# Performance work log

Measured on AMD Instinct MI355X. Metric: run time of the kernel, lower is better.

Reference implementation:

```python
import jax, jax.numpy as jnp
import numpy as np

D = 512; N_HEAD = 8; D_HEAD = 64; D_INNER = 2048; SEG = 512; N_LAYER = 2; BATCH = 32
NUM_ITEMS = 50000
OMEGA = [2, 3, 4, 5, 7, 11, 21, 50]  # len == N_HEAD, required by multi-scale mask broadcast
EPS = 1e-8
STD = 0.02


def _layer_norm(x, w, b):
    mu = x.mean(-1, keepdims=True)
    var = ((x - mu) ** 2).mean(-1, keepdims=True)
    return (x - mu) / jnp.sqrt(var + EPS) * w + b


def _masks():
    # dir_mask: triu(ones, 1) (reverse=False); ms_mask[i,j,m] per omega band
    dir_mask = jnp.triu(jnp.ones((SEG, SEG), jnp.float32), 1)
    ms = np.stack([np.tri(SEG, SEG, o - 1) != np.tri(SEG, SEG, -o) for o in OMEGA], axis=-1)
    return dir_mask, jnp.asarray(ms)


def _pos_emb():
    freq = jnp.arange(0, D, 2, dtype=jnp.float32)
    inv_freq = 1.0 / jnp.power(10000.0, freq / D)
    pos_seq = jnp.arange(SEG, -SEG, -1.0, dtype=jnp.float32)  # length 2*SEG
    sinusoid = pos_seq[:, None] * inv_freq[None, :]
    return jnp.concatenate([jnp.sin(sinusoid), jnp.cos(sinusoid)], axis=-1)  # (2S, D)


def _rel_shift_bnij(x, klen):
    b, n, i, j2 = x.shape
    x = x.reshape(b, n, j2, i)[:, :, 1:, :].reshape(b, n, i, j2 - 1)
    return x[:, :, :, :klen]


def setup_inputs() -> dict:
    key = jax.random.key(0)
    ks = jax.random.split(key, 16)
    L = N_LAYER
    item_emb = STD * jax.random.normal(ks[0], (NUM_ITEMS + 1, D), jnp.float32)
    item_emb = item_emb.at[0].set(0.0)  # padding_idx=0
    proj = lambda k: STD * jax.random.normal(k, (L, D, N_HEAD, D_HEAD), jnp.float32)
    return {
        "input_ids": jax.random.randint(ks[1], (BATCH, SEG), 0, NUM_ITEMS + 1),
        "input_mask": jnp.zeros((BATCH, SEG), jnp.float32),
        "item_emb": item_emb,
        "Wq": proj(ks[2]), "Wk": proj(ks[3]), "Wv": proj(ks[4]),
        "Wr": proj(ks[5]), "Wo": proj(ks[6]),
        "r_r_bias": STD * jax.random.normal(ks[7], (L, N_HEAD, D_HEAD), jnp.float32),
        "r_w_bias": STD * jax.random.normal(ks[8], (L, N_HEAD, D_HEAD), jnp.float32),
        "ln_attn_w": jnp.ones((L, D), jnp.float32), "ln_attn_b": jnp.zeros((L, D), jnp.float32),
        "W1": STD * jax.random.normal(ks[9], (L, D, D_INNER), jnp.float32),
        "b1": jnp.zeros((L, D_INNER), jnp.float32),
        "W2": STD * jax.random.normal(ks[10], (L, D_INNER, D), jnp.float32),
        "b2": jnp.zeros((L, D), jnp.float32),
        "ln_ff_w": jnp.ones((L, D), jnp.float32), "ln_ff_b": jnp.zeros((L, D), jnp.float32),
    }


def reference(input_ids, input_mask, item_emb, Wq, Wk, Wv, Wr, Wo, r_r_bias, r_w_bias,
              ln_attn_w, ln_attn_b, W1, b1, W2, b2, ln_ff_w, ln_ff_b):
    ids = input_ids.T                      # (S, B)
    im = input_mask.T.astype(jnp.float32)  # (S, B)
    dir_mask, ms_mask = _masks()
    # data_mask: (q,k,b); attn_mask: (q,k,b,n) via multi-scale bands (training path)
    data_mask = im[None, :, :] + im[:, None, :] + dir_mask[:, :, None]
    attn_mask = ((data_mask[:, :, :, None] + (~ms_mask)[:, :, None, :].astype(jnp.float32)) > 0).astype(jnp.float32)
    mask_bnij = jnp.transpose(attn_mask, (2, 3, 0, 1))  # (b,n,i,j)

    h = item_emb[ids]          # (S, B, D)
    pos = _pos_emb()           # (2S, D), shared across batch
    scale = 1.0 / np.sqrt(D_HEAD).astype(np.float32)

    for l in range(N_LAYER):
        k_h = jnp.einsum('ibh,hnd->ibnd', h, Wk[l])
        v_h = jnp.einsum('ibh,hnd->ibnd', h, Wv[l])
        k_r = jnp.einsum('jh,hnd->jnd', pos, Wr[l])   # pos shared across batch
        q_h = jnp.einsum('ibh,hnd->ibnd', h, Wq[l])
        ac = jnp.einsum('ibnd,jbnd->bnij', q_h + r_w_bias[l], k_h)
        bd = jnp.einsum('ibnd,jnd->bnij', q_h + r_r_bias[l], k_r)
        bd = _rel_shift_bnij(bd, SEG)
        attn_score = (ac + bd) * scale - 1e30 * mask_bnij
        attn_prob = jax.nn.softmax(attn_score, axis=3)
        attn_vec = jnp.einsum('bnij,jbnd->ibnd', attn_prob, v_h)
        attn_out = jnp.einsum('ibnd,hnd->ibh', attn_vec, Wo[l])
        h = _layer_norm(attn_out + h, ln_attn_w[l], ln_attn_b[l])
        ff = jax.nn.gelu(h @ W1[l] + b1[l], approximate=False) @ W2[l] + b2[l]
        h = _layer_norm(ff + h, ln_ff_w[l], ln_ff_b[l])

    return jnp.transpose(h, (1, 0, 2))  # (B, S, D)
```

## Files before the change

### kernel.cpp

```cpp
#include <hip/hip_runtime.h>
#include <math.h>


#define S_  512
#define B_  32
#define D_  512
#define NH  8
#define DH  64
#define DI  2048
#define M_  (S_*B_)
#define QKV_LD 1536
#define WL  3407872
#define FP32_ONE 0x3F800000u

typedef unsigned short ushort_t;
typedef __attribute__((ext_vector_type(8))) short short8;
typedef __attribute__((ext_vector_type(4))) float f32x4;

__constant__ int OMEGA_C[8] = {2, 3, 4, 5, 7, 11, 21, 50};

__device__ __forceinline__ float b2f(ushort_t us) {
    return __uint_as_float(((unsigned int)us) << 16);
}
__device__ __forceinline__ ushort_t f2b(float f) {
    unsigned int u = __float_as_uint(f);
    return (ushort_t)((u + 0x7fffu + ((u >> 16) & 1u)) >> 16);
}
__device__ __forceinline__ float ldx(const void* p, size_t idx, bool isbf) {
    return isbf ? b2f(((const ushort_t*)p)[idx]) : ((const float*)p)[idx];
}
__device__ __forceinline__ void async16(const ushort_t* g, ushort_t* l) {
    __builtin_amdgcn_global_load_lds(
        (const __attribute__((address_space(1))) unsigned int*)g,
        (__attribute__((address_space(3))) unsigned int*)l, 16, 0, 0);
}

__device__ __forceinline__ float fast_gelu(float v) {
    float x  = v * 0.7071067811865475f;
    float ax = fabsf(x);
    float t  = __builtin_amdgcn_rcpf(fmaf(0.3275911f, ax, 1.f));
    float p  = fmaf(fmaf(fmaf(fmaf(1.061405429f, t, -1.453152027f),
                              t, 1.421413741f),
                         t, -0.284496736f),
                    t, 0.254829592f) * t;
    float e    = __expf(-ax * ax);
    float erfa = fmaf(-p, e, 1.f);
    float erfx = copysignf(erfa, x);
    return 0.5f * v * (1.f + erfx);
}

#define DPPA(v, ctrl) v += __int_as_float(__builtin_amdgcn_update_dpp(0, __float_as_int(v), ctrl, 0xf, 0xf, true))
__device__ __forceinline__ void dpp_sum64(float& v) {
    DPPA(v, 0x111); DPPA(v, 0x112); DPPA(v, 0x114);
    DPPA(v, 0x118); DPPA(v, 0x142); DPPA(v, 0x143);
}
#define DPPROR(v, ctrl) __int_as_float(__builtin_amdgcn_update_dpp(__float_as_int(v), __float_as_int(v), ctrl, 0xf, 0xf, false))
__device__ __forceinline__ float row16_sum(float v) {
    v += DPPROR(v, 0x128); v += DPPROR(v, 0x124);
    v += DPPROR(v, 0x122); v += DPPROR(v, 0x121);
    return v;
}
__device__ __forceinline__ float row16_max(float v) {
    v = fmaxf(v, DPPROR(v, 0x128)); v = fmaxf(v, DPPROR(v, 0x124));
    v = fmaxf(v, DPPROR(v, 0x122)); v = fmaxf(v, DPPROR(v, 0x121));
    return v;
}
__device__ __forceinline__ float rlane(float v, int l) {
    return __int_as_float(__builtin_amdgcn_readlane(__float_as_int(v), l));
}

__global__ __launch_bounds__(256) void embed_kernel(const int* __restrict__ ids,
                                                    const void* __restrict__ emb,
                                                    ushort_t* __restrict__ h,
                                                    const unsigned int* __restrict__ dtp) {
    const bool isbf = (dtp[0] != FP32_ONE);
    int idx = blockIdx.x * 256 + threadIdx.x;
    int d8 = idx & 63;
    int row = idx >> 6;
    int s = row >> 5, b = row & 31;
    int id = ids[b * S_ + s];
    size_t src = (size_t)id * D_ + d8 * 8;
    if (isbf) {
        *(uint4*)(h + (size_t)row * D_ + d8 * 8) = *(const uint4*)((const ushort_t*)emb + src);
    } else {
        const float* e = (const float*)emb + src;
        float4 a0 = ((const float4*)e)[0], a1 = ((const float4*)e)[1];
        uint4 pk;
        pk.x = (unsigned)f2b(a0.x) | ((unsigned)f2b(a0.y) << 16);
        pk.y = (unsigned)f2b(a0.z) | ((unsigned)f2b(a0.w) << 16);
        pk.z = (unsigned)f2b(a1.x) | ((unsigned)f2b(a1.y) << 16);
        pk.w = (unsigned)f2b(a1.z) | ((unsigned)f2b(a1.w) << 16);
        *(uint4*)(h + (size_t)row * D_ + d8 * 8) = pk;
    }
}

__global__ __launch_bounds__(256) void posemb_kernel(ushort_t* __restrict__ pos) {
    int flat = blockIdx.x * 256 + threadIdx.x;
    int p = flat >> 8, k = flat & 255;
    float inv = expf((float)k * -0.035977892078031f);
    float val = (512.0f - (float)p) * inv;
    pos[p * D_ + k]       = f2b(sinf(val));
    pos[p * D_ + 256 + k] = f2b(cosf(val));
}

__global__ __launch_bounds__(256) void transp_cvt4(
    const void* __restrict__ s0, const void* __restrict__ s1,
    const void* __restrict__ s2, const void* __restrict__ s3,
    ushort_t* __restrict__ wbuf, const unsigned int* __restrict__ dtp) {
    const bool isbf = (dtp[0] != FP32_ONE);
    __shared__ float tt[32][33];
    int z = blockIdx.z, layer = z >> 2, t4 = z & 3;
    const void* srcs[4] = {s0, s1, s2, s3};
    const void* in = srcs[t4];
    size_t inoff = (size_t)layer * 262144;
    ushort_t* out = wbuf + (size_t)layer * WL + (size_t)t4 * 262144;
    int tx = threadIdx.x & 31, ty = threadIdx.x >> 5;
    int n0 = blockIdx.x * 32, k0 = blockIdx.y * 32;
#pragma unroll
    for (int it = 0; it < 4; ++it)
        tt[ty + it * 8][tx] = ldx(in, inoff + (size_t)(k0 + ty + it * 8) * 512 + n0 + tx, isbf);
    __syncthreads();
#pragma unroll
    for (int it = 0; it < 4; ++it)
        out[(size_t)(n0 + ty + it * 8) * 512 + k0 + tx] = f2b(tt[tx][ty + it * 8]);
}

__global__ __launch_bounds__(256) void transp_cvtL(const void* __restrict__ in, size_t perlin,
                                                   ushort_t* __restrict__ wbuf, size_t outoff,
                                                   const unsigned int* __restrict__ dtp,
                                                   int K, int N) {
    const bool isbf = (dtp[0] != FP32_ONE);
    __shared__ float tt[32][33];
    int layer = blockIdx.z;
    size_t inoff = (size_t)layer * perlin;
    ushort_t* out = wbuf + (size_t)layer * WL + outoff;
    int tx = threadIdx.x & 31, ty = threadIdx.x >> 5;
    int n0 = blockIdx.x * 32, k0 = blockIdx.y * 32;
#pragma unroll
    for (int it = 0; it < 4; ++it)
        tt[ty + it * 8][tx] = ldx(in, inoff + (size_t)(k0 + ty + it * 8) * N + n0 + tx, isbf);
    __syncthreads();
#pragma unroll
    for (int it = 0; it < 4; ++it)
        out[(size_t)(n0 + ty + it * 8) * K + k0 + tx] = f2b(tt[tx][ty + it * 8]);
}

__global__ __launch_bounds__(256) void cvtL(const void* __restrict__ in, size_t perlin,
                                            ushort_t* __restrict__ wbuf, size_t outoff,
                                            const unsigned int* __restrict__ dtp, int nelem) {
    const bool isbf = (dtp[0] != FP32_ONE);
    int layer = blockIdx.z;
    int i = blockIdx.x * 256 + threadIdx.x;
    if (i < nelem)
        wbuf[(size_t)layer * WL + outoff + i] = f2b(ldx(in, (size_t)layer * perlin + i, isbf));
}

template<int EPI>
__global__ __launch_bounds__(512)
void mfma_gemm(const ushort_t* __restrict__ A, int lda,
               const ushort_t* __restrict__ Bt, int ldb,
               const void* __restrict__ biasv, size_t biasoff,
               ushort_t* __restrict__ C, int ldc,
               size_t bzoff, size_t czoff,
               const unsigned int* __restrict__ dtp, int M, int N, int K) {
    const bool isbf = (dtp[0] != FP32_ONE);
    __shared__ ushort_t As[2][128 * 32];
    __shared__ ushort_t Bs[2][128 * 32];
    const int tid = threadIdx.x;
    Bt += (size_t)blockIdx.z * bzoff;
    C  += (size_t)blockIdx.z * czoff;
    const int nwg = gridDim.x * gridDim.y;
    const int wg  = blockIdx.y * gridDim.x + blockIdx.x;
    const int cpx = nwg >> 3;
    const int swz = (wg & 7) * cpx + (wg >> 3);
    const int bm = (swz / gridDim.y) * 128;
    const int bn = (swz % gridDim.y) * 128;
    const int w = tid >> 6, lane = tid & 63;
    const int wr = w >> 2, wc = w & 3;
    const int quad = lane >> 4, l16 = lane & 15;
    const int fsw  = (l16 >> 1) & 3;

    const int srow = tid >> 2;
    const int ssw  = (srow >> 1) & 3;
    const int sck  = (tid & 3) ^ ssw;
    const ushort_t* gA = A  + (size_t)(bm + srow) * lda + sck * 8;
    const ushort_t* gB = Bt + (size_t)(bn + srow) * ldb + sck * 8;
    const int ldst = tid * 8;

#define STAGE_T(kt, bi) do {                                  \
        int _k0 = (kt) << 5;                                  \
        async16(gA + _k0, As[bi] + ldst);                     \
        async16(gB + _k0, Bs[bi] + ldst);                     \
    } while (0)

    f32x4 acc[4][2];
#pragma unroll
    for (int i = 0; i < 4; ++i)
#pragma unroll
        for (int j = 0; j < 2; ++j)
#pragma unroll
            for (int r = 0; r < 4; ++r) acc[i][j][r] = 0.f;

    const int nt = K >> 5;
    STAGE_T(0, 0);
    STAGE_T(1, 1);
    for (int t = 0; t < nt; ++t) {
        const int cur = t & 1;
        if (t + 1 < nt) asm volatile("s_waitcnt vmcnt(2)" ::: "memory");
        else            asm volatile("s_waitcnt vmcnt(0)" ::: "memory");
        __builtin_amdgcn_s_barrier();
        asm volatile("" ::: "memory");

        short8 af[4], bf[2];
#pragma unroll
        for (int tt = 0; tt < 4; ++tt) {
            int ra = wr * 64 + tt * 16 + l16;
            af[tt] = *(const short8*)(As[cur] + ra * 32 + ((quad ^ fsw) * 8));
        }
#pragma unroll
        for (int tc = 0; tc < 2; ++tc) {
            int rb = wc * 32 + tc * 16 + l16;
            bf[tc] = *(const short8*)(Bs[cur] + rb * 32 + ((quad ^ fsw) * 8));
        }
#pragma unroll
        for (int tr = 0; tr < 4; ++tr)
#pragma unroll
            for (int tc = 0; tc < 2; ++tc)
                acc[tr][tc] = __builtin_amdgcn_mfma_f32_16x16x32_bf16(bf[tc], af[tr], acc[tr][tc], 0, 0, 0);

        asm volatile("s_waitcnt lgkmcnt(0)" ::: "memory");
        __builtin_amdgcn_s_barrier();
        if (t + 2 < nt) STAGE_T(t + 2, cur);
    }
#undef STAGE_T

    float bv[2][4];
    if (EPI >= 1) {
#pragma unroll
        for (int tc = 0; tc < 2; ++tc)
#pragma unroll
            for (int r = 0; r < 4; ++r)
                bv[tc][r] = ldx(biasv, biasoff + bn + wc * 32 + tc * 16 + quad * 4 + r, isbf);
    }
#pragma unroll
    for (int tr = 0; tr < 4; ++tr) {
        int grow = bm + wr * 64 + tr * 16 + l16;
#pragma unroll
        for (int tc = 0; tc < 2; ++tc) {
            int gcb = bn + wc * 32 + tc * 16 + quad * 4;
            float x[4];
#pragma unroll
            for (int r = 0; r < 4; ++r) {
                float v = acc[tr][tc][r];
                if (EPI >= 1) v += bv[tc][r];
                if (EPI == 2) v = fast_gelu(v);
                x[r] = v;
            }
            uint2 pk;
            pk.x = (unsigned)f2b(x[0]) | ((unsigned)f2b(x[1]) << 16);
            pk.y = (unsigned)f2b(x[2]) | ((unsigned)f2b(x[3]) << 16);
            *(uint2*)(C + (size_t)grow * ldc + gcb) = pk;
        }
    }
}

__global__ __launch_bounds__(256) void attn_mfma(
    ushort_t* __restrict__ qkv, const ushort_t* __restrict__ krb,
    const void* __restrict__ rwb, const void* __restrict__ rrb, size_t boff,
    const void* __restrict__ im,
    const unsigned int* __restrict__ dtp) {
    const bool isbf = (dtp[0] != FP32_ONE);
    __shared__ ushort_t Ks[128 * 64];
    __shared__ ushort_t VT[64 * 128];
    __shared__ ushort_t Rs[64 * 64];
    __shared__ float    BD2[4 * 16 * 64];
    __shared__ ushort_t Ps[4 * 16 * 128];
    __shared__ float    imk[128];
    __shared__ float    imq[64];

    const int tid = threadIdx.x;
    const int bid  = (blockIdx.z * gridDim.y + blockIdx.y) * gridDim.x + blockIdx.x;
    const int xcd  = bid & 7, slot = bid >> 3;
    const int i0 = (slot & 7) * 64;
    const int n  = (slot >> 3) & 7;
    const int b  = xcd * 4 + (slot >> 6);
    const int o  = OMEGA_C[n];
    const int noff = n * DH;
    const int j0 = i0 - 64;
    const int w = tid >> 6, lane = tid & 63;
    const int quad = lane >> 4, l16 = lane & 15;

#pragma unroll
    for (int it = 0; it < 4; ++it) {
        int q4 = it * 256 + tid;
        int c  = q4 >> 3, ch = q4 & 7;
        int jc = j0 + c; jc = jc < 0 ? 0 : jc;
        size_t rowb = (size_t)(jc * B_ + b) * QKV_LD + noff;
        *(uint4*)(Ks + c * 64 + ((ch ^ (c & 7)) << 3)) = *(const uint4*)(qkv + rowb + 512 + ch * 8);
        ushort_t v8[8];
        *(uint4*)v8 = *(const uint4*)(qkv + rowb + 1024 + ch * 8);
#pragma unroll
        for (int e = 0; e < 8; ++e) {
            int vr = ch * 8 + e;
            VT[vr * 128 + (((c >> 3) ^ (vr & 15)) << 3) + (c & 7)] = v8[e];
        }
    }
#pragma unroll
    for (int it = 0; it < 2; ++it) {
        int q4 = it * 256 + tid;
        int m = q4 >> 3, ch = q4 & 7;
        *(uint4*)(Rs + m * 64 + ((ch ^ (m & 7)) << 3)) =
            *(const uint4*)(krb + (size_t)(512 - m) * 512 + noff + ch * 8);
    }
    if (tid < 128) {
        int j = j0 + tid;
        imk[tid] = (j >= 0) ? ldx(im, b * S_ + j, isbf) : 0.f;
    } else if (tid < 192) {
        imq[tid - 128] = ldx(im, b * S_ + i0 + (tid - 128), isbf);
    }
    __syncthreads();

    const int qrow = i0 + w * 16 + l16;
    size_t qbase = (size_t)(qrow * B_ + b) * QKV_LD + noff;
    short8 aw[2], ar[2];
#pragma unroll
    for (int kc = 0; kc < 2; ++kc) {
        int kof = kc * 32 + quad * 8;
        ushort_t qe[8];
        *(uint4*)qe = *(const uint4*)(qkv + qbase + kof);
#pragma unroll
        for (int e = 0; e < 8; ++e) {
            float f = b2f(qe[e]);
            ((ushort_t*)&aw[kc])[e] = f2b(f + ldx(rwb, boff + noff + kof + e, isbf));
            ((ushort_t*)&ar[kc])[e] = f2b(f + ldx(rrb, boff + noff + kof + e, isbf));
        }
    }

    f32x4 accs[8];
#pragma unroll
    for (int ct = 0; ct < 8; ++ct) {
        int kr = ct * 16 + l16;
        short8 b0 = *(const short8*)(Ks + kr * 64 + ((quad ^ (kr & 7)) << 3));
        short8 b1 = *(const short8*)(Ks + kr * 64 + (((quad + 4) ^ (kr & 7)) << 3));
        f32x4 z = {0.f, 0.f, 0.f, 0.f};
        z = __builtin_amdgcn_mfma_f32_16x16x32_bf16(aw[0], b0, z, 0, 0, 0);
        z = __builtin_amdgcn_mfma_f32_16x16x32_bf16(aw[1], b1, z, 0, 0, 0);
        accs[ct] = z;
    }
    float* BD2w = BD2 + w * 16 * 64;
#pragma unroll
    for (int mt = 0; mt < 4; ++mt) {
        int rr = mt * 16 + l16;
        short8 b0 = *(const short8*)(Rs + rr * 64 + ((quad ^ (rr & 7)) << 3));
        short8 b1 = *(const short8*)(Rs + rr * 64 + (((quad + 4) ^ (rr & 7)) << 3));
        f32x4 z = {0.f, 0.f, 0.f, 0.f};
        z = __builtin_amdgcn_mfma_f32_16x16x32_bf16(ar[0], b0, z, 0, 0, 0);
        z = __builtin_amdgcn_mfma_f32_16x16x32_bf16(ar[1], b1, z, 0, 0, 0);
#pragma unroll
        for (int r = 0; r < 4; ++r)
            BD2w[(quad * 4 + r) * 64 + mt * 16 + l16] = z[r];
    }

    float im_i[4];
#pragma unroll
    for (int r = 0; r < 4; ++r) im_i[r] = imq[w * 16 + quad * 4 + r];

    float sc[8][4];
#pragma unroll
    for (int ct = 0; ct < 8; ++ct) {
        int cl = ct * 16 + l16;
        float imk_c = imk[cl];
#pragma unroll
        for (int r = 0; r < 4; ++r) {
            int qrl = w * 16 + quad * 4 + r;
            int rel = qrl + 64 - cl;
            int relc = rel < 0 ? 0 : (rel > 63 ? 63 : rel);
            float bd = BD2w[(quad * 4 + r) * 64 + relc];
            bool valid = (rel >= 0) && (rel < o) && (rel <= i0 + qrl)
                         && (im_i[r] + imk_c <= 0.f);
            sc[ct][r] = valid ? (accs[ct][r] + bd) * 0.125f : -1e30f;
        }
    }
    float rl[4];
#pragma unroll
    for (int r = 0; r < 4; ++r) {
        float mx = sc[0][r];
#pragma unroll
        for (int ct = 1; ct < 8; ++ct) mx = fmaxf(mx, sc[ct][r]);
        mx = row16_max(mx);
        float l = 0.f;
#pragma unroll
        for (int ct = 0; ct < 8; ++ct) {
            float pv = __expf(sc[ct][r] - mx);
            sc[ct][r] = pv;
            l += pv;
        }
        l = row16_sum(l);
        rl[r] = 1.f / l;
    }
    ushort_t* Pw = Ps + w * 16 * 128;
#pragma unroll
    for (int ct = 0; ct < 8; ++ct)
#pragma unroll
        for (int r = 0; r < 4; ++r) {
            int prow = quad * 4 + r;
            Pw[prow * 128 + ((((ct * 2 + (l16 >> 3)) ^ prow) & 15) << 3) + (l16 & 7)]
                = f2b(sc[ct][r] * rl[r]);
        }

    short8 aP[4];
#pragma unroll
    for (int kc = 0; kc < 4; ++kc)
        aP[kc] = *(const short8*)(Pw + l16 * 128 + ((((kc * 4 + quad) ^ l16) & 15) << 3));

    const int qg = i0 + w * 16 + l16;
    const size_t obase = (size_t)(qg * B_ + b) * QKV_LD + noff;
#pragma unroll
    for (int dt = 0; dt < 4; ++dt) {
        f32x4 accT = {0.f, 0.f, 0.f, 0.f};
#pragma unroll
        for (int kc = 0; kc < 4; ++kc) {
            int vrow = dt * 16 + l16;
            short8 bV = *(const short8*)(VT + vrow * 128 + ((((kc * 4 + quad) ^ (vrow & 15)) & 15) << 3));
            accT = __builtin_amdgcn_mfma_f32_16x16x32_bf16(bV, aP[kc], accT, 0, 0, 0);
        }
        uint2 pk;
        pk.x = (unsigned)f2b(accT[0]) | ((unsigned)f2b(accT[1]) << 16);
        pk.y = (unsigned)f2b(accT[2]) | ((unsigned)f2b(accT[3]) << 16);
        *(uint2*)(qkv + obase + dt * 16 + quad * 4) = pk;
    }
}

__global__ __launch_bounds__(256) void add_ln_kernel(
    const ushort_t* __restrict__ x, ushort_t* __restrict__ h,
    const void* __restrict__ w, const void* __restrict__ b, size_t boff,
    const unsigned int* __restrict__ dtp) {
    const bool isbf = (dtp[0] != FP32_ONE);
    int lane = threadIdx.x & 63;
    int row = blockIdx.x * 4 + (threadIdx.x >> 6);
    size_t base = (size_t)row * D_ + lane * 8;
    ushort_t xe[8], he[8];
    *(uint4*)xe = *(const uint4*)(x + base);
    *(uint4*)he = *(const uint4*)(h + base);
    float v[8];
    float s = 0.f, ss = 0.f;
#pragma unroll
    for (int e = 0; e < 8; ++e) {
        v[e] = b2f(xe[e]) + b2f(he[e]);
        s += v[e]; ss += v[e] * v[e];
    }
    dpp_sum64(s); dpp_sum64(ss);
    float S = rlane(s, 63), SS = rlane(ss, 63);
    float mu  = S * (1.f / D_);
    float var = fmaxf(SS * (1.f / D_) - mu * mu, 0.f);
    float inv = rsqrtf(var + 1e-8f);
    ushort_t oe[8];
#pragma unroll
    for (int e = 0; e < 8; ++e)
        oe[e] = f2b((v[e] - mu) * inv * ldx(w, boff + lane * 8 + e, isbf)
                    + ldx(b, boff + lane * 8 + e, isbf));
    *(uint4*)(h + base) = *(uint4*)oe;
}

__global__ __launch_bounds__(256) void writeout_kernel(const ushort_t* __restrict__ h,
                                                       void* __restrict__ out,
                                                       const unsigned int* __restrict__ dtp) {
    const bool isbf = (dtp[0] != FP32_ONE);
    int idx = blockIdx.x * 256 + threadIdx.x;
    int d8 = idx & 63;
    int rest = idx >> 6;
    int s = rest & (S_ - 1), b = rest >> 9;
    ushort_t ve[8];
    *(uint4*)ve = *(const uint4*)(h + ((size_t)(s * B_ + b) << 9) + d8 * 8);
    if (isbf) {
        *(uint4*)((ushort_t*)out + (size_t)idx * 8) = *(uint4*)ve;
    } else {
        float* op = (float*)out + (size_t)idx * 8;
        ((float4*)op)[0] = make_float4(b2f(ve[0]), b2f(ve[1]), b2f(ve[2]), b2f(ve[3]));
        ((float4*)op)[1] = make_float4(b2f(ve[4]), b2f(ve[5]), b2f(ve[6]), b2f(ve[7]));
    }
}

extern "C" void kernel_launch(void* const* d_in, const int* in_sizes, int n_in,
                              void* d_out, int out_size, void* d_ws, size_t ws_size,
                              hipStream_t stream) {
    (void)in_sizes; (void)n_in; (void)out_size; (void)ws_size;
    const int*  ids = (const int*)d_in[0];
    const void* im  = d_in[1];
    const void* emb = d_in[2];
    const void* Wq = d_in[3], *Wk = d_in[4], *Wv = d_in[5], *Wr = d_in[6], *Wo = d_in[7];
    const void* rrb = d_in[8], *rwb = d_in[9];
    const void* lnaw = d_in[10], *lnab = d_in[11];
    const void* W1 = d_in[12], *b1 = d_in[13], *W2 = d_in[14], *b2 = d_in[15];
    const void* lnfw = d_in[16], *lnfb = d_in[17];
    const unsigned int* dtp = (const unsigned int*)d_in[10];

    char* wsb = (char*)d_ws;
    ushort_t* h    = (ushort_t*)wsb;
    ushort_t* qkv  = (ushort_t*)(wsb + (16u << 20));
    ushort_t* tmp  = (ushort_t*)(wsb + (64u << 20));
    ushort_t* ff1  = (ushort_t*)(wsb + (80u << 20));
    ushort_t* wbuf = (ushort_t*)(wsb + (144u << 20));
    ushort_t* posb = (ushort_t*)(wsb + (157u << 20));
    ushort_t* krb0 = (ushort_t*)(wsb + (158u << 20));
    ushort_t* krb1 = (ushort_t*)(wsb + (159u << 20));

    embed_kernel<<<4096, 256, 0, stream>>>(ids, emb, h, dtp);
    posemb_kernel<<<1024, 256, 0, stream>>>(posb);

    transp_cvt4<<<dim3(16, 16, 8), 256, 0, stream>>>(Wq, Wk, Wv, Wr, wbuf, dtp);
    cvtL<<<dim3(1024, 1, 2), 256, 0, stream>>>(Wo, 262144, wbuf, 1048576, dtp, 262144);
    transp_cvtL<<<dim3(64, 16, 2), 256, 0, stream>>>(W1, 1048576, wbuf, 1310720, dtp, 512, 2048);
    transp_cvtL<<<dim3(16, 64, 2), 256, 0, stream>>>(W2, 1048576, wbuf, 2359296, dtp, 2048, 512);

    mfma_gemm<0><<<dim3(8, 4, 2), 512, 0, stream>>>(posb, 512, wbuf + 786432, 512, nullptr, 0,
                                                    krb0, 512, WL, 524288, dtp, 1024, 512, 512);

    for (int l = 0; l < 2; ++l) {
        size_t boff = (size_t)l * 512;
        size_t b1off = (size_t)l * 2048;
        ushort_t* qkvT = wbuf + (size_t)l * WL;
        ushort_t* woc  = qkvT + 1048576;
        ushort_t* w1T  = woc  + 262144;
        ushort_t* w2T  = w1T  + 1048576;
        ushort_t* krb  = l ? krb1 : krb0;

        mfma_gemm<0><<<dim3(128, 12), 512, 0, stream>>>(h, 512, qkvT, 512, nullptr, 0, qkv, QKV_LD, 0, 0, dtp, M_, QKV_LD, 512);

        attn_mfma<<<dim3(8, 32, 8), 256, 0, stream>>>(qkv, krb, rwb, rrb, boff, im, dtp);

        mfma_gemm<0><<<dim3(128, 4), 512, 0, stream>>>(qkv, QKV_LD, woc, 512, nullptr, 0, tmp, 512, 0, 0, dtp, M_, 512, 512);
        add_ln_kernel<<<4096, 256, 0, stream>>>(tmp, h, lnaw, lnab, boff, dtp);

        mfma_gemm<2><<<dim3(128, 16), 512, 0, stream>>>(h, 512, w1T, 512, b1, b1off, ff1, DI, 0, 0, dtp, M_, DI, 512);
        mfma_gemm<1><<<dim3(128, 4),  512, 0, stream>>>(ff1, DI, w2T, 2048, b2, boff, tmp, 512, 0, 0, dtp, M_, 512, DI);
        add_ln_kernel<<<4096, 256, 0, stream>>>(tmp, h, lnfw, lnfb, boff, dtp);
    }

    writeout_kernel<<<4096, 256, 0, stream>>>(h, d_out, dtp);
}
```

Baseline: 726.8 us.

## Shrink attention LDS footprint via buffer aliasing and split K/V layouts

Removes the shared-memory copy of the relative-position keys and reads them straight from global memory in the BD matmul. The per-wave BD scratch and the probability tile now share one buffer with a padded row stride of 66. K and V^T are split into 32-wide halves and quarters with new XOR swizzles. The aim is to cut LDS use per block so more blocks fit per CU, and to reduce bank conflicts, at the cost of uncached global reads for R.

After: 747.6 us. 1.03x slower.

```diff
diff --git a/kernel.cpp b/kernel.cpp
--- a/kernel.cpp
+++ b/kernel.cpp
@@ -270,11 +270,9 @@
     const void* __restrict__ im,
     const unsigned int* __restrict__ dtp) {
     const bool isbf = (dtp[0] != FP32_ONE);
-    __shared__ ushort_t Ks[128 * 64];
-    __shared__ ushort_t VT[64 * 128];
-    __shared__ ushort_t Rs[64 * 64];
-    __shared__ float    BD2[4 * 16 * 64];
-    __shared__ ushort_t Ps[4 * 16 * 128];
+    __shared__ ushort_t Ks[2][128 * 32];
+    __shared__ ushort_t VT[4][64 * 32];
+    __shared__ float    SCR[4 * 1056];
     __shared__ float    imk[128];
     __shared__ float    imq[64];
 
@@ -296,21 +294,22 @@
         int c  = q4 >> 3, ch = q4 & 7;
         int jc = j0 + c; jc = jc < 0 ? 0 : jc;
         size_t rowb = (size_t)(jc * B_ + b) * QKV_LD + noff;
-        *(uint4*)(Ks + c * 64 + ((ch ^ (c & 7)) << 3)) = *(const uint4*)(qkv + rowb + 512 + ch * 8);
+        {
+            int hh = ch >> 2, lc = ch & 3;
+            int ph = lc ^ ((c >> 1) & 3);
+            *(uint4*)(Ks[hh] + c * 32 + ph * 8) = *(const uint4*)(qkv + rowb + 512 + ch * 8);
+        }
         ushort_t v8[8];
         *(uint4*)v8 = *(const uint4*)(qkv + rowb + 1024 + ch * 8);
-#pragma unroll
-        for (int e = 0; e < 8; ++e) {
-            int vr = ch * 8 + e;
-            VT[vr * 128 + (((c >> 3) ^ (vr & 15)) << 3) + (c & 7)] = v8[e];
-        }
-    }
-#pragma unroll
-    for (int it = 0; it < 2; ++it) {
-        int q4 = it * 256 + tid;
-        int m = q4 >> 3, ch = q4 & 7;
-        *(uint4*)(Rs + m * 64 + ((ch ^ (m & 7)) << 3)) =
-            *(const uint4*)(krb + (size_t)(512 - m) * 512 + noff + ch * 8);
+        {
+            int a = c >> 5, lj = (c >> 3) & 3, off = c & 7;
+#pragma unroll
+            for (int e = 0; e < 8; ++e) {
+                int vr = ch * 8 + e;
+                int ph = lj ^ ((vr >> 1) & 3) ^ ((vr >> 3) & 3);
+                VT[a][vr * 32 + ph * 8 + off] = v8[e];
+            }
+        }
     }
     if (tid < 128) {
         int j = j0 + tid;
@@ -340,25 +339,27 @@
 #pragma unroll
     for (int ct = 0; ct < 8; ++ct) {
         int kr = ct * 16 + l16;
-        short8 b0 = *(const short8*)(Ks + kr * 64 + ((quad ^ (kr & 7)) << 3));
-        short8 b1 = *(const short8*)(Ks + kr * 64 + (((quad + 4) ^ (kr & 7)) << 3));
+        int ph = quad ^ ((kr >> 1) & 3);
+        short8 b0 = *(const short8*)(Ks[0] + kr * 32 + ph * 8);
+        short8 b1 = *(const short8*)(Ks[1] + kr * 32 + ph * 8);
         f32x4 z = {0.f, 0.f, 0.f, 0.f};
         z = __builtin_amdgcn_mfma_f32_16x16x32_bf16(aw[0], b0, z, 0, 0, 0);
         z = __builtin_amdgcn_mfma_f32_16x16x32_bf16(aw[1], b1, z, 0, 0, 0);
         accs[ct] = z;
     }
-    float* BD2w = BD2 + w * 16 * 64;
+    float* BD2w = SCR + w * 1056;
 #pragma unroll
     for (int mt = 0; mt < 4; ++mt) {
         int rr = mt * 16 + l16;
-        short8 b0 = *(const short8*)(Rs + rr * 64 + ((quad ^ (rr & 7)) << 3));
-        short8 b1 = *(const short8*)(Rs + rr * 64 + (((quad + 4) ^ (rr & 7)) << 3));
+        const ushort_t* rrow = krb + (size_t)(512 - rr) * 512 + noff;
+        short8 b0 = *(const short8*)(rrow + quad * 8);
+        short8 b1 = *(const short8*)(rrow + 32 + quad * 8);
         f32x4 z = {0.f, 0.f, 0.f, 0.f};
         z = __builtin_amdgcn_mfma_f32_16x16x32_bf16(ar[0], b0, z, 0, 0, 0);
         z = __builtin_amdgcn_mfma_f32_16x16x32_bf16(ar[1], b1, z, 0, 0, 0);
 #pragma unroll
         for (int r = 0; r < 4; ++r)
-            BD2w[(quad * 4 + r) * 64 + mt * 16 + l16] = z[r];
+            BD2w[(quad * 4 + r) * 66 + mt * 16 + l16] = z[r];
     }
 
     float im_i[4];
@@ -375,7 +376,7 @@
             int qrl = w * 16 + quad * 4 + r;
             int rel = qrl + 64 - cl;
             int relc = rel < 0 ? 0 : (rel > 63 ? 63 : rel);
-            float bd = BD2w[(quad * 4 + r) * 64 + relc];
+            float bd = BD2w[(quad * 4 + r) * 66 + relc];
             bool valid = (rel >= 0) && (rel < o) && (rel <= i0 + qrl)
                          && (im_i[r] + imk_c <= 0.f);
             sc[ct][r] = valid ? (accs[ct][r] + bd) * 0.125f : -1e30f;
@@ -398,7 +399,7 @@
         l = row16_sum(l);
         rl[r] = 1.f / l;
     }
-    ushort_t* Pw = Ps + w * 16 * 128;
+    ushort_t* Pw = (ushort_t*)(SCR + w * 1056);
 #pragma unroll
     for (int ct = 0; ct < 8; ++ct)
 #pragma unroll
@@ -421,7 +422,8 @@
 #pragma unroll
         for (int kc = 0; kc < 4; ++kc) {
             int vrow = dt * 16 + l16;
-            short8 bV = *(const short8*)(VT + vrow * 128 + ((((kc * 4 + quad) ^ (vrow & 15)) & 15) << 3));
+            int ph = quad ^ ((vrow >> 1) & 3) ^ ((vrow >> 3) & 3);
+            short8 bV = *(const short8*)(VT[kc] + vrow * 32 + ph * 8);
             accT = __builtin_amdgcn_mfma_f32_16x16x32_bf16(bV, aP[kc], accT, 0, 0, 0);
         }
         uint2 pk;
```
